# Optimization experiments

Hardware: AMD Instinct MI355X
Metric: run time of the kernel (lower is better)

Reference implementation:

```python
import jax, jax.numpy as jnp
import numpy as np

# Static architecture constants (match init_kwargs)
N, M, DIM = 2048, 4096, 256
KS = (0.9, 0.8, 0.7)
HEADS, BOT_HEADS = 4, 2
NEG_SLOPE = 0.2  # PyG GATConv default leaky-relu slope


def _p(key, shape, scale):
    return (scale * jax.random.normal(key, shape, dtype=jnp.float32))


def setup_inputs() -> dict:
    key = jax.random.key(0)
    ks = jax.random.split(key, 16)
    # Symmetric positive connectivity matrix (fMRI-like), fully dense
    R = jax.random.uniform(ks[0], (N, N), dtype=jnp.float32)
    A = 0.5 * (R + R.T)
    X = jax.random.normal(ks[1], (N, DIM), dtype=jnp.float32)
    s = 1.0 / np.sqrt(DIM).astype(np.float32)
    C, Cb = DIM // HEADS, DIM // BOT_HEADS
    inp = {
        'A': A, 'X': X,
        'W_down': _p(ks[2], (3, DIM, DIM), s),
        'as_down': _p(ks[3], (3, HEADS, C), s),
        'ad_down': _p(ks[4], (3, HEADS, C), s),
        'b_down': jnp.zeros((3, DIM), jnp.float32),
        'W_up': _p(ks[5], (3, DIM, DIM), s),
        'as_up': _p(ks[6], (3, HEADS, C), s),
        'ad_up': _p(ks[7], (3, HEADS, C), s),
        'b_up': jnp.zeros((3, DIM), jnp.float32),
        'W_bot': _p(ks[8], (DIM, DIM), s),
        'as_bot': _p(ks[9], (BOT_HEADS, Cb), s),
        'ad_bot': _p(ks[10], (BOT_HEADS, Cb), s),
        'b_bot': jnp.zeros((DIM,), jnp.float32),
        'W_pool': _p(ks[11], (3, DIM), s),
        'b_pool': jnp.zeros((3,), jnp.float32),
        'W_ups': _p(ks[12], (M, N), 1.0 / np.sqrt(N).astype(np.float32)),
        'b_ups': jnp.zeros((M,), jnp.float32),
    }
    return inp


def _sym_norm(A):
    # A_tilde = A + I ; D^{-1/2} A_tilde D^{-1/2} as elementwise broadcast
    A = A + jnp.eye(A.shape[0], dtype=A.dtype)
    d = A.sum(axis=1) + 1e-5
    di = d ** -0.5
    return di[:, None] * A * di[None, :]


def _gat(A, X, W, a_src, a_dst, b):
    # Dense-masked GATConv (concat=True, eval mode => no dropout).
    # Edge j->i exists iff A[j, i] > 0 (dense_to_sparse row=src, col=tgt).
    n = X.shape[0]
    H, C = a_src.shape
    x = (X @ W).reshape(n, H, C)                       # [n, H, C]
    s = jnp.einsum('nhc,hc->nh', x, a_src)             # source logit term
    t = jnp.einsum('nhc,hc->nh', x, a_dst)             # target logit term
    logits = jax.nn.leaky_relu(t[:, None, :] + s[None, :, :], NEG_SLOPE)  # [i, j, h]
    mask = (A.T > 0)[:, :, None]
    attn = jax.nn.softmax(jnp.where(mask, logits, -jnp.inf), axis=1)
    out = jnp.einsum('ijh,jhc->ihc', attn, x).reshape(n, H * C) + b
    return jax.nn.relu(out)


def reference(A, X, W_down, as_down, ad_down, b_down,
              W_up, as_up, ad_up, b_up,
              W_bot, as_bot, ad_bot, b_bot,
              W_pool, b_pool, W_ups, b_ups):
    A = _sym_norm(A)
    A_hist, idx_hist = [], []
    # Encoder: GAT -> top-k pool (gather rows/cols)
    for i in range(3):
        X = _gat(A, X, W_down[i], as_down[i], ad_down[i], b_down[i])
        A_hist.append(A)
        scores = jax.nn.sigmoid(X @ W_pool[i] + b_pool[i])
        k = max(2, int(KS[i] * A.shape[0]))            # static sizes
        vals, idx = jax.lax.top_k(scores, k)
        X = X[idx] * vals[:, None]
        A = A[idx][:, idx]
        idx_hist.append(idx)
    X = _gat(A, X, W_bot, as_bot, ad_bot, b_bot)
    # Decoder: scatter-unpool -> GAT -> adjacency reconstruction
    for i in range(3):
        u = 2 - i
        A, idx = A_hist[u], idx_hist[u]
        Xn = jnp.zeros((A.shape[0], X.shape[1]), X.dtype).at[idx].set(X)
        X = _gat(A, Xn, W_up[i], as_up[i], ad_up[i], b_up[i])
    # Upsampler: Linear(n->m) on X^T, then A_up = relu(Xu Xu^T)
    X_up = W_ups @ X + b_ups[:, None]                  # [M, DIM]
    A_up = jax.nn.relu(X_up @ X_up.T)                  # [M, M]
    return A_up
```

## Files before the change

### kernel.cpp

```cpp
#include <hip/hip_runtime.h>
#include <math.h>

#define NEG 0.2f
#define NMAX 2048
#define CHUNK 64
#define NCHMAX 32

__device__ __forceinline__ float lrelu(float v) { return v > 0.f ? v : NEG * v; }
__device__ __forceinline__ unsigned fenc(float v) {
    unsigned u = __float_as_uint(v);
    return (u & 0x80000000u) ? ~u : (u | 0x80000000u);
}
__device__ __forceinline__ float fdec(unsigned u) {
    return (u & 0x80000000u) ? __uint_as_float(u ^ 0x80000000u) : __uint_as_float(~u);
}

__global__ __launch_bounds__(256) void gemm_ks(const float* __restrict__ A,
                                               const float* __restrict__ B,
                                               float* __restrict__ C,
                                               const int* __restrict__ rowmapA,
                                               const float* __restrict__ rowscale,
                                               const int* __restrict__ rowmapC,
                                               int M, int N, int K) {
    __shared__ float As[16][68];
    __shared__ float Bs[16][68];
    const int tid = threadIdx.x;
    const int m0 = blockIdx.x * 64, n0 = blockIdx.y * 64;
    const int kchunk = K / gridDim.z;
    const int kbeg = blockIdx.z * kchunk, kend = kbeg + kchunk;
    const int tm = tid >> 4, tn = tid & 15;
    const int lr = tid >> 2, lc4 = (tid & 3) * 4;
    const int br = tid >> 4, bc4 = (tid & 15) * 4;
    const int am = m0 + lr;
    const bool aval = am < M;
    int arow = 0; float ascale = 1.f;
    if (aval) { arow = rowmapA ? rowmapA[am] : am; if (rowscale) ascale = rowscale[arow]; }
    const float* Ap = A + (size_t)arow * K;
    float4 va = make_float4(0.f, 0.f, 0.f, 0.f), vb;
    if (aval) va = *(const float4*)(Ap + kbeg + lc4);
    vb = *(const float4*)(B + (size_t)(kbeg + br) * N + n0 + bc4);
    float acc[4][4] = {{0.f}};
    for (int k0 = kbeg; k0 < kend; k0 += 16) {
        As[lc4 + 0][lr] = va.x * ascale; As[lc4 + 1][lr] = va.y * ascale;
        As[lc4 + 2][lr] = va.z * ascale; As[lc4 + 3][lr] = va.w * ascale;
        *(float4*)&Bs[br][bc4] = vb;
        __syncthreads();
        if (k0 + 16 < kend) {
            if (aval) va = *(const float4*)(Ap + k0 + 16 + lc4);
            vb = *(const float4*)(B + (size_t)(k0 + 16 + br) * N + n0 + bc4);
        }
#pragma unroll
        for (int kk = 0; kk < 16; ++kk) {
            float a[4], b[4];
            *(float4*)a = *(const float4*)&As[kk][tm * 4];
            *(float4*)b = *(const float4*)&Bs[kk][tn * 4];
#pragma unroll
            for (int x = 0; x < 4; ++x)
#pragma unroll
                for (int y = 0; y < 4; ++y) acc[x][y] = fmaf(a[x], b[y], acc[x][y]);
        }
        __syncthreads();
    }
#pragma unroll
    for (int x = 0; x < 4; ++x) {
        int m = m0 + tm * 4 + x;
        if (m >= M) continue;
        int orow = rowmapC ? rowmapC[m] : m;
        float* dst = C + (size_t)orow * N + n0 + tn * 4;
#pragma unroll
        for (int y = 0; y < 4; ++y) atomicAdd(dst + y, acc[x][y]);
    }
}

__global__ __launch_bounds__(256) void st_kernel(const float* __restrict__ xw,
                                                 const float* __restrict__ asrc,
                                                 const float* __restrict__ adst,
                                                 float* __restrict__ S, float* __restrict__ T,
                                                 unsigned* __restrict__ SMX,
                                                 int n, int Hh, int Cc) {
    int gid = blockIdx.x * 256 + threadIdx.x;
    int i = gid / Hh, h = gid - i * Hh;
    float s = -INFINITY;
    if (i < n) {
        const float* xr = xw + (size_t)i * 256 + h * Cc;
        const float* pa = asrc + h * Cc;
        const float* pd = adst + h * Cc;
        float sv = 0.f, tv = 0.f;
        for (int c = 0; c < Cc; c += 4) {
            float4 xv = *(const float4*)(xr + c);
            float4 av = *(const float4*)(pa + c);
            float4 dv = *(const float4*)(pd + c);
            sv += xv.x * av.x + xv.y * av.y + xv.z * av.z + xv.w * av.w;
            tv += xv.x * dv.x + xv.y * dv.y + xv.z * dv.z + xv.w * dv.w;
        }
        S[(size_t)i * Hh + h] = sv;
        T[(size_t)i * Hh + h] = tv;
        s = sv;
    }
    for (int off = Hh; off < 64; off <<= 1) s = fmaxf(s, __shfl_xor(s, off));
    int lane = threadIdx.x & 63;
    if (lane < Hh && s > -INFINITY) atomicMax(SMX + lane, fenc(s));
}

__global__ __launch_bounds__(256) void rank_k(const float* __restrict__ S,
                                              float* __restrict__ SS, int* __restrict__ PERM,
                                              int n, int Hh) {
    __shared__ float s[NMAX];
    int h = blockIdx.y;
    for (int j = threadIdx.x; j < n; j += 256) s[j] = S[(size_t)j * Hh + h];
    __syncthreads();
    int i = blockIdx.x * 256 + threadIdx.x;
    if (i >= n) return;
    float v = s[i];
    int cnt = 0, j = 0;
    for (; j + 4 <= n; j += 4) {
        float4 sv = *(const float4*)&s[j];
        cnt += (sv.x > v) || (sv.x == v && (j + 0) < i);
        cnt += (sv.y > v) || (sv.y == v && (j + 1) < i);
        cnt += (sv.z > v) || (sv.z == v && (j + 2) < i);
        cnt += (sv.w > v) || (sv.w == v && (j + 3) < i);
    }
    for (; j < n; ++j) {
        float sj = s[j];
        cnt += (sj > v) || (sj == v && j < i);
    }
    SS[h * NMAX + cnt] = v;
    PERM[h * NMAX + cnt] = i;
}

__global__ __launch_bounds__(256) void chunk_k(const float* __restrict__ XW,
                                               const float* __restrict__ SS,
                                               const int* __restrict__ PERM,
                                               const unsigned* __restrict__ SMX,
                                               float* __restrict__ TOT1, float* __restrict__ TOT2,
                                               float* __restrict__ ZT1, float* __restrict__ ZT2,
                                               int n, int Cc) {
    const int h = blockIdx.x, ch = blockIdx.y;
    const int nh = 256 / Cc, seg = CHUNK / nh;
    const int c = threadIdx.x % Cc, half = threadIdx.x / Cc;
    __shared__ float ssh[CHUNK];
    __shared__ int pjh[CHUNK];
    __shared__ float red1[256], red2[256];
    __shared__ float zr1[4], zr2[4];
    if (threadIdx.x < CHUNK) {
        int rk = ch * CHUNK + threadIdx.x;
        ssh[threadIdx.x] = (rk < n) ? SS[h * NMAX + rk] : 0.f;
        pjh[threadIdx.x] = (rk < n) ? PERM[h * NMAX + rk] : -1;
    }
    __syncthreads();
    const float smax = fdec(SMX[h]);
    float t1 = 0.f, t2 = 0.f, z1 = 0.f, z2 = 0.f;
#pragma unroll 4
    for (int q = 0; q < seg; ++q) {
        int r = half * seg + q;
        int j = pjh[r];
        if (j < 0) continue;
        float d = ssh[r] - smax;
        float w1 = expf(d), w2 = expf(NEG * d);
        float x = XW[(size_t)j * 256 + h * Cc + c];
        t1 = fmaf(w1, x, t1); t2 = fmaf(w2, x, t2);
        z1 += w1; z2 += w2;
    }
    red1[threadIdx.x] = t1; red2[threadIdx.x] = t2;
    if (c == 0) { zr1[half] = z1; zr2[half] = z2; }
    __syncthreads();
    if (half == 0) {
        for (int hh = 1; hh < nh; ++hh) { t1 += red1[hh * Cc + c]; t2 += red2[hh * Cc + c]; }
        TOT1[((size_t)h * NCHMAX + ch) * Cc + c] = t1;
        TOT2[((size_t)h * NCHMAX + ch) * Cc + c] = t2;
        if (c == 0) {
            float a = z1, b = z2;
            for (int hh = 1; hh < nh; ++hh) { a += zr1[hh]; b += zr2[hh]; }
            ZT1[h * NCHMAX + ch] = a;
            ZT2[h * NCHMAX + ch] = b;
        }
    }
}

__global__ __launch_bounds__(256) void combine_k(
    const float* __restrict__ XW, const float* __restrict__ SS,
    const int* __restrict__ PERM, const unsigned* __restrict__ SMX,
    const float* __restrict__ T,
    const float* __restrict__ TOT1, const float* __restrict__ TOT2,
    const float* __restrict__ ZT1, const float* __restrict__ ZT2,
    const float* __restrict__ bias, const float* __restrict__ Wp,
    const float* __restrict__ bp,
    float* __restrict__ Xout, float* __restrict__ SC, int n, int Hh, int nch) {
    const int i = blockIdx.x, t = threadIdx.x;
    const int C = 256 / Hh;
    __shared__ float f1s[4], f2s[4], invs[4], smaxs[4];
    __shared__ int qs[4], chs[4];
    __shared__ float coef[256];
    __shared__ int permsh[256];
    __shared__ float redw[4];
    float z1p = 0.f, z2s = 0.f;
    if (t < Hh) {
        int h = t;
        float smax = fdec(SMX[h]);
        smaxs[h] = smax;
        float tv = T[(size_t)i * Hh + h];
        float u = tv + smax, m = lrelu(u);
        f1s[h] = expf(u - m);
        f2s[h] = expf(NEG * u - m);
        float thr = -tv;
        int lo = 0, hi = n;
        while (lo < hi) {
            int mid = (lo + hi) >> 1;
            if (SS[h * NMAX + mid] > thr) lo = mid + 1; else hi = mid;
        }
        int q = lo;
        int ch = min(q / CHUNK, nch - 1);
        qs[h] = q; chs[h] = ch;
        for (int cc = 0; cc < ch; ++cc) z1p += ZT1[h * NCHMAX + cc];
        for (int cc = ch + 1; cc < nch; ++cc) z2s += ZT2[h * NCHMAX + cc];
    }
    __syncthreads();
    if (t < Hh * CHUNK) {
        int h = t >> 6, r = t & 63;
        int rank = chs[h] * CHUNK + r;
        float w = 0.f; int j = 0;
        if (rank < n) {
            float ssv = SS[h * NMAX + rank];
            j = PERM[h * NMAX + rank];
            float d = ssv - smaxs[h];
            w = (rank < qs[h]) ? f1s[h] * expf(d) : f2s[h] * expf(NEG * d);
        }
        coef[t] = w; permsh[t] = j;
    }
    __syncthreads();
    if (t < Hh) {
        int h = t;
        float den = fmaf(f1s[h], z1p, f2s[h] * z2s);
        for (int r = 0; r < CHUNK; ++r) den += coef[h * CHUNK + r];
        invs[h] = 1.f / den;
    }
    __syncthreads();
    const int h = t / C, c = t - h * C;
    const float* xcol = XW + h * C + c;
    float csum = 0.f;
#pragma unroll 8
    for (int r = 0; r < CHUNK; ++r)
        csum = fmaf(coef[h * CHUNK + r], xcol[(size_t)permsh[h * CHUNK + r] * 256], csum);
    float a1 = 0.f, a2 = 0.f;
    const int ch = chs[h];
    for (int cc = 0; cc < ch; ++cc) a1 += TOT1[((size_t)h * NCHMAX + cc) * C + c];
    for (int cc = ch + 1; cc < nch; ++cc) a2 += TOT2[((size_t)h * NCHMAX + cc) * C + c];
    float out = (fmaf(f1s[h], a1, f2s[h] * a2) + csum) * invs[h] + bias[t];
    out = fmaxf(out, 0.f);
    Xout[(size_t)i * 256 + t] = out;
    if (Wp) {
        float v = out * Wp[t];
#pragma unroll
        for (int off = 32; off; off >>= 1) v += __shfl_xor(v, off);
        if ((t & 63) == 0) redw[t >> 6] = v;
        __syncthreads();
        if (t == 0)
            SC[i] = 1.f / (1.f + expf(-(redw[0] + redw[1] + redw[2] + redw[3] + bp[0])));
    }
}

__global__ __launch_bounds__(256) void topk_k(const float* __restrict__ SC,
                                              int* __restrict__ IDX, int n, int k) {
    __shared__ float s[NMAX];
    for (int j = threadIdx.x; j < n; j += 256) s[j] = SC[j];
    __syncthreads();
    int i = blockIdx.x * 256 + threadIdx.x;
    if (i >= n) return;
    float v = s[i];
    int cnt = 0, j = 0;
    for (; j + 4 <= n; j += 4) {
        float4 sv = *(const float4*)&s[j];
        cnt += (sv.x > v) || (sv.x == v && (j + 0) < i);
        cnt += (sv.y > v) || (sv.y == v && (j + 1) < i);
        cnt += (sv.z > v) || (sv.z == v && (j + 2) < i);
        cnt += (sv.w > v) || (sv.w == v && (j + 3) < i);
    }
    for (; j < n; ++j) {
        float sj = s[j];
        cnt += (sj > v) || (sj == v && j < i);
    }
    if (cnt < k) IDX[cnt] = i;
}

__global__ __launch_bounds__(256) void ttr_sym(const float* __restrict__ A,
                                               const float* __restrict__ bias,
                                               float* __restrict__ C, int M, int K) {
    const int L = blockIdx.x;
    int by = (int)((sqrtf(8.f * L + 1.f) - 1.f) * 0.5f);
    while ((by + 1) * (by + 2) / 2 <= L) ++by;
    while (by * (by + 1) / 2 > L) --by;
    const int bx = L - by * (by + 1) / 2;
    __shared__ float As[16][132];
    __shared__ float Bs[16][132];
    const int tid = threadIdx.x;
    const int m0 = bx * 128, n0 = by * 128;
    const int lr = tid >> 1, lc8 = (tid & 1) * 8;
    const int tm = tid >> 4, tn = tid & 15;
    const float ab = bias[m0 + lr], bb = bias[n0 + lr];
    const float* Ar = A + (size_t)(m0 + lr) * K;
    const float* Br = A + (size_t)(n0 + lr) * K;
    float4 va0 = *(const float4*)(Ar + lc8), va1 = *(const float4*)(Ar + lc8 + 4);
    float4 vb0 = *(const float4*)(Br + lc8), vb1 = *(const float4*)(Br + lc8 + 4);
    float acc[8][8] = {{0.f}};
    for (int k0 = 0; k0 < K; k0 += 16) {
        As[lc8 + 0][lr] = va0.x + ab; As[lc8 + 1][lr] = va0.y + ab;
        As[lc8 + 2][lr] = va0.z + ab; As[lc8 + 3][lr] = va0.w + ab;
        As[lc8 + 4][lr] = va1.x + ab; As[lc8 + 5][lr] = va1.y + ab;
        As[lc8 + 6][lr] = va1.z + ab; As[lc8 + 7][lr] = va1.w + ab;
        Bs[lc8 + 0][lr] = vb0.x + bb; Bs[lc8 + 1][lr] = vb0.y + bb;
        Bs[lc8 + 2][lr] = vb0.z + bb; Bs[lc8 + 3][lr] = vb0.w + bb;
        Bs[lc8 + 4][lr] = vb1.x + bb; Bs[lc8 + 5][lr] = vb1.y + bb;
        Bs[lc8 + 6][lr] = vb1.z + bb; Bs[lc8 + 7][lr] = vb1.w + bb;
        __syncthreads();
        if (k0 + 16 < K) {
            va0 = *(const float4*)(Ar + k0 + 16 + lc8); va1 = *(const float4*)(Ar + k0 + 20 + lc8);
            vb0 = *(const float4*)(Br + k0 + 16 + lc8); vb1 = *(const float4*)(Br + k0 + 20 + lc8);
        }
#pragma unroll
        for (int kk = 0; kk < 16; ++kk) {
            float a[8], b[8];
            *(float4*)&a[0] = *(const float4*)&As[kk][tm * 4];
            *(float4*)&a[4] = *(const float4*)&As[kk][64 + tm * 4];
            *(float4*)&b[0] = *(const float4*)&Bs[kk][tn * 4];
            *(float4*)&b[4] = *(const float4*)&Bs[kk][64 + tn * 4];
#pragma unroll
            for (int x = 0; x < 8; ++x)
#pragma unroll
                for (int y = 0; y < 8; ++y) acc[x][y] = fmaf(a[x], b[y], acc[x][y]);
        }
        __syncthreads();
    }
#pragma unroll
    for (int x = 0; x < 8; ++x)
#pragma unroll
        for (int y = 0; y < 8; ++y) acc[x][y] = fmaxf(acc[x][y], 0.f);
#pragma unroll
    for (int x = 0; x < 8; ++x) {
        int row = m0 + ((x < 4) ? tm * 4 + x : 64 + tm * 4 + (x - 4));
        float* dst = C + (size_t)row * M + n0;
        *(float4*)(dst + tn * 4) = make_float4(acc[x][0], acc[x][1], acc[x][2], acc[x][3]);
        *(float4*)(dst + 64 + tn * 4) = make_float4(acc[x][4], acc[x][5], acc[x][6], acc[x][7]);
    }
    if (bx != by) {
#pragma unroll
        for (int y = 0; y < 8; ++y) {
            int row = n0 + ((y < 4) ? tn * 4 + y : 64 + tn * 4 + (y - 4));
            float* dst = C + (size_t)row * M + m0;
            *(float4*)(dst + tm * 4) = make_float4(acc[0][y], acc[1][y], acc[2][y], acc[3][y]);
            *(float4*)(dst + 64 + tm * 4) = make_float4(acc[4][y], acc[5][y], acc[6][y], acc[7][y]);
        }
    }
}

extern "C" void kernel_launch(void* const* d_in, const int* in_sizes, int n_in,
                              void* d_out, int out_size, void* d_ws, size_t ws_size,
                              hipStream_t stream) {
    const float* X0      = (const float*)d_in[1];
    const float* W_down  = (const float*)d_in[2];
    const float* as_down = (const float*)d_in[3];
    const float* ad_down = (const float*)d_in[4];
    const float* b_down  = (const float*)d_in[5];
    const float* W_up    = (const float*)d_in[6];
    const float* as_up   = (const float*)d_in[7];
    const float* ad_up   = (const float*)d_in[8];
    const float* b_up    = (const float*)d_in[9];
    const float* W_bot   = (const float*)d_in[10];
    const float* as_bot  = (const float*)d_in[11];
    const float* ad_bot  = (const float*)d_in[12];
    const float* b_bot   = (const float*)d_in[13];
    const float* W_pool  = (const float*)d_in[14];
    const float* b_pool  = (const float*)d_in[15];
    const float* W_ups   = (const float*)d_in[16];
    const float* b_ups   = (const float*)d_in[17];
    float* out = (float*)d_out;

    float* F = (float*)d_ws;
    size_t o = 0;
    float* Xb  = F + o; o += 2048 * 256;
    float* XW  = F + o; o += 2048 * 256;
    unsigned* SMX = (unsigned*)(F + o); o += 16;
    float* S   = F + o; o += 2048 * 4;
    float* T   = F + o; o += 2048 * 4;
    float* SS  = F + o; o += 2048 * 4;
    int* PERM  = (int*)(F + o); o += 2048 * 4;
    float* TOT1 = F + o; o += 8192;
    float* TOT2 = F + o; o += 8192;
    float* ZT1 = F + o; o += 128;
    float* ZT2 = F + o; o += 128;
    float* SC  = F + o; o += 2048;
    int* IDXs[3];
    IDXs[0] = (int*)(F + o); o += 2048;
    IDXs[1] = (int*)(F + o); o += 2048;
    IDXs[2] = (int*)(F + o); o += 2048;
    float* XU  = F + o; o += 4096 * 256;

    auto cdiv = [](int a, int b) { return (a + b - 1) / b; };

    auto run_gat = [&](const float* Xin, int Mrows, int n, const float* W,
                       const float* asrc, const float* adst, const float* bias, int Hh,
                       const int* rmA, const float* rscale, const int* rmC,
                       const float* Wp, const float* bp) {
        int C = 256 / Hh;
        int nch = cdiv(n, CHUNK);
        hipMemsetAsync(XW, 0, (size_t)(2048 * 256 + 16) * 4, stream);
        gemm_ks<<<dim3(cdiv(Mrows, 64), 4, 4), 256, 0, stream>>>(Xin, W, XW, rmA, rscale,
                                                                 rmC, Mrows, 256, 256);
        st_kernel<<<cdiv(n * Hh, 256), 256, 0, stream>>>(XW, asrc, adst, S, T, SMX, n, Hh, C);
        rank_k<<<dim3(cdiv(n, 256), Hh), 256, 0, stream>>>(S, SS, PERM, n, Hh);
        chunk_k<<<dim3(Hh, nch), 256, 0, stream>>>(XW, SS, PERM, SMX, TOT1, TOT2, ZT1, ZT2,
                                                   n, C);
        combine_k<<<n, 256, 0, stream>>>(XW, SS, PERM, SMX, T, TOT1, TOT2, ZT1, ZT2, bias,
                                         Wp, bp, Xb, SC, n, Hh, nch);
    };

    const int ns[4] = {2048, 1843, 1474, 1031};

    for (int l = 0; l < 3; ++l) {
        int n = ns[l], k = ns[l + 1];
        run_gat(l ? Xb : X0, n, n, W_down + (size_t)l * 65536, as_down + l * 256,
                ad_down + l * 256, b_down + l * 256, 4,
                l ? IDXs[l - 1] : nullptr, l ? SC : nullptr, nullptr,
                W_pool + l * 256, b_pool + l);
        topk_k<<<cdiv(n, 256), 256, 0, stream>>>(SC, IDXs[l], n, k);
    }

    run_gat(Xb, ns[3], ns[3], W_bot, as_bot, ad_bot, b_bot, 2, IDXs[2], SC, nullptr,
            nullptr, nullptr);

    for (int i = 0; i < 3; ++i) {
        int u = 2 - i;
        int pn = ns[u], kc = ns[u + 1];
        run_gat(Xb, kc, pn, W_up + (size_t)i * 65536, as_up + i * 256, ad_up + i * 256,
                b_up + i * 256, 4, nullptr, nullptr, IDXs[u], nullptr, nullptr);
    }

    hipMemsetAsync(XU, 0, (size_t)4096 * 256 * 4, stream);
    gemm_ks<<<dim3(64, 4, 4), 256, 0, stream>>>(W_ups, Xb, XU, nullptr, nullptr, nullptr,
                                                4096, 256, 2048);
    ttr_sym<<<528, 256, 0, stream>>>(XU, b_ups, out, 4096, 256);
}
```

Before: 1.183 ms.

## Fuse each GAT layer and upsampler into persistent kernels with grid barriers

Replaces the per-layer sequence of gemm, score, rank, chunk and combine launches, plus the top-k and memsets, with one persistent kernel per GAT layer that uses software grid-wide barriers between phases. The up-path scatter is replaced by an inverse-index gather. S/T logit computation is fused into the GEMM epilogue, and split-K atomics are replaced by direct stores. Softmax max now comes from the sorted array instead of an atomic max. The upsampler GEMM and the symmetric relu(XXᵀ) are also fused into a single persistent kernel with larger 128x128 tiles. This aims to cut launch overhead and memset/atomic traffic, at the risk of deadlock if not all 512 blocks are co-resident, and barrier spin cost.

After: 3.206 ms. +171.1%, slower.

```diff
diff --git a/kernel.cpp b/kernel.cpp
--- a/kernel.cpp
+++ b/kernel.cpp
@@ -5,349 +5,447 @@
 #define NMAX 2048
 #define CHUNK 64
 #define NCHMAX 32
+#define GRID 512
 
 __device__ __forceinline__ float lrelu(float v) { return v > 0.f ? v : NEG * v; }
-__device__ __forceinline__ unsigned fenc(float v) {
-    unsigned u = __float_as_uint(v);
-    return (u & 0x80000000u) ? ~u : (u | 0x80000000u);
+
+__device__ __forceinline__ void gsync(unsigned* c, unsigned nb) {
+    __syncthreads();
+    if (threadIdx.x == 0) {
+        __threadfence();
+        atomicAdd(c, 1u);
+        while (__hip_atomic_load(c, __ATOMIC_ACQUIRE, __HIP_MEMORY_SCOPE_AGENT) < nb) {
+            __builtin_amdgcn_s_sleep(2);
+        }
+        __threadfence();
+    }
+    __syncthreads();
 }
-__device__ __forceinline__ float fdec(unsigned u) {
-    return (u & 0x80000000u) ? __uint_as_float(u ^ 0x80000000u) : __uint_as_float(~u);
+
+struct GatArgs {
+    const float* Xin; const float* W; float* XW;
+    const int* rowmapA; const float* rowscale;
+    const float* asrc; const float* adst;
+    float* S; float* T; float* SS; int* PERM;
+    float* TOT1; float* TOT2; float* ZT1; float* ZT2;
+    const float* bias; const float* Wp; const float* bp;
+    float* Xout; float* SC;
+    const float* tkSC; int* tkIDX; int* tkINV; int tkN; int tkK;
+    unsigned* bar;
+    int n; int Hh;
+};
+
+union SharedU {
+    struct { float As[16][68], Bs[16][68], Sred[64][17], Tred[64][17]; } g;
+    struct { float s[NMAX]; } rk;
+    struct { float ssh[CHUNK]; int pjh[CHUNK]; float red1[256], red2[256], zr1[4], zr2[4]; } ck;
+    struct { float f1s[4], f2s[4], invs[4], smaxs[4]; int qs[4], chs[4];
+             float coef[256]; int permsh[256]; float redw[4]; } cb;
+    struct { float sc[NMAX]; } tk;
+};
+
+__global__ __launch_bounds__(256, 2) void gat_fused(GatArgs a) {
+    __shared__ SharedU sh;
+    const int tid = threadIdx.x;
+    const int nb = gridDim.x, bid = blockIdx.x;
+    const int n = a.n, Hh = a.Hh, Cc = 256 / Hh;
+    unsigned* bar = a.bar;
+    int slot = 0;
+
+    if (a.tkIDX) {
+        for (int base = bid * 256; base < a.tkN; base += nb * 256) {
+            for (int j = tid; j < a.tkN; j += 256) sh.tk.sc[j] = a.tkSC[j];
+            __syncthreads();
+            int i = base + tid;
+            if (i < a.tkN) {
+                float v = sh.tk.sc[i];
+                int cnt = 0, j = 0;
+                for (; j + 4 <= a.tkN; j += 4) {
+                    float4 sv = *(const float4*)&sh.tk.sc[j];
+                    cnt += (sv.x > v) || (sv.x == v && (j + 0) < i);
+                    cnt += (sv.y > v) || (sv.y == v && (j + 1) < i);
+                    cnt += (sv.z > v) || (sv.z == v && (j + 2) < i);
+                    cnt += (sv.w > v) || (sv.w == v && (j + 3) < i);
+                }
+                for (; j < a.tkN; ++j) {
+                    float sj = sh.tk.sc[j];
+                    cnt += (sj > v) || (sj == v && j < i);
+                }
+                if (cnt < a.tkK) { a.tkIDX[cnt] = i; a.tkINV[i] = cnt; }
+                else a.tkINV[i] = -1;
+            }
+            __syncthreads();
+        }
+    }
+    gsync(bar + slot++, nb);
+
+    {
+        const int mt = (n + 63) >> 6;
+        for (int tt = bid; tt < mt * 4; tt += nb) {
+            const int m0 = (tt >> 2) * 64, n0 = (tt & 3) * 64;
+            const int tm = tid >> 4, tn = tid & 15;
+            const int lr = tid >> 2, lc4 = (tid & 3) * 4;
+            const int br = tid >> 4, bc4 = (tid & 15) * 4;
+            const int am = m0 + lr;
+            bool aval = am < n;
+            int arow = am; float ascale = 1.f;
+            if (aval && a.rowmapA) { arow = a.rowmapA[am]; if (arow < 0) { aval = false; arow = 0; } }
+            if (aval && a.rowscale) ascale = a.rowscale[arow];
+            const float* Ap = a.Xin + (size_t)arow * 256;
+            float4 va = make_float4(0.f, 0.f, 0.f, 0.f);
+            if (aval) va = *(const float4*)(Ap + lc4);
+            float4 vb = *(const float4*)(a.W + (size_t)br * 256 + n0 + bc4);
+            float acc[4][4] = {{0.f}};
+            for (int k0 = 0; k0 < 256; k0 += 16) {
+                sh.g.As[lc4 + 0][lr] = va.x * ascale; sh.g.As[lc4 + 1][lr] = va.y * ascale;
+                sh.g.As[lc4 + 2][lr] = va.z * ascale; sh.g.As[lc4 + 3][lr] = va.w * ascale;
+                *(float4*)&sh.g.Bs[br][bc4] = vb;
+                __syncthreads();
+                if (k0 + 16 < 256) {
+                    if (aval) va = *(const float4*)(Ap + k0 + 16 + lc4);
+                    vb = *(const float4*)(a.W + (size_t)(k0 + 16 + br) * 256 + n0 + bc4);
+                }
+#pragma unroll
+                for (int kk = 0; kk < 16; ++kk) {
+                    float aa[4], bb[4];
+                    *(float4*)aa = *(const float4*)&sh.g.As[kk][tm * 4];
+                    *(float4*)bb = *(const float4*)&sh.g.Bs[kk][tn * 4];
+#pragma unroll
+                    for (int x = 0; x < 4; ++x)
+#pragma unroll
+                        for (int y = 0; y < 4; ++y) acc[x][y] = fmaf(aa[x], bb[y], acc[x][y]);
+                }
+                __syncthreads();
+            }
+#pragma unroll
+            for (int x = 0; x < 4; ++x) {
+                int m = m0 + tm * 4 + x;
+                if (m < n)
+                    *(float4*)(a.XW + (size_t)m * 256 + n0 + tn * 4) =
+                        make_float4(acc[x][0], acc[x][1], acc[x][2], acc[x][3]);
+            }
+            if (Hh == 4) {
+                const int h = tt & 3;
+                float4 a4 = *(const float4*)(a.asrc + h * 64 + tn * 4);
+                float4 d4 = *(const float4*)(a.adst + h * 64 + tn * 4);
+#pragma unroll
+                for (int x = 0; x < 4; ++x) {
+                    sh.g.Sred[tm * 4 + x][tn] = acc[x][0] * a4.x + acc[x][1] * a4.y +
+                                                acc[x][2] * a4.z + acc[x][3] * a4.w;
+                    sh.g.Tred[tm * 4 + x][tn] = acc[x][0] * d4.x + acc[x][1] * d4.y +
+                                                acc[x][2] * d4.z + acc[x][3] * d4.w;
+                }
+                __syncthreads();
+                if (tid < 64) {
+                    int m = m0 + tid;
+                    if (m < n) {
+                        float s = 0.f, t = 0.f;
+#pragma unroll
+                        for (int q = 0; q < 16; ++q) { s += sh.g.Sred[tid][q]; t += sh.g.Tred[tid][q]; }
+                        a.S[(size_t)m * Hh + h] = s;
+                        a.T[(size_t)m * Hh + h] = t;
+                    }
+                }
+                __syncthreads();
+            }
+        }
+    }
+    gsync(bar + slot++, nb);
+
+    if (Hh == 2) {
+        for (int gid = bid * 256 + tid; gid < n * 2; gid += nb * 256) {
+            int i = gid >> 1, h = gid & 1;
+            const float* xr = a.XW + (size_t)i * 256 + h * 128;
+            const float* pa = a.asrc + h * 128;
+            const float* pd = a.adst + h * 128;
+            float sv = 0.f, tv = 0.f;
+            for (int c = 0; c < 128; c += 4) {
+                float4 xv = *(const float4*)(xr + c);
+                float4 av = *(const float4*)(pa + c);
+                float4 dv = *(const float4*)(pd + c);
+                sv += xv.x * av.x + xv.y * av.y + xv.z * av.z + xv.w * av.w;
+                tv += xv.x * dv.x + xv.y * dv.y + xv.z * dv.z + xv.w * dv.w;
+            }
+            a.S[(size_t)i * 2 + h] = sv;
+            a.T[(size_t)i * 2 + h] = tv;
+        }
+        gsync(bar + slot++, nb);
+    }
+
+    {
+        const int nseg = (n + 255) >> 8;
+        for (int w = bid; w < Hh * nseg; w += nb) {
+            const int h = w / nseg, seg = w - h * nseg;
+            for (int j = tid; j < n; j += 256) sh.rk.s[j] = a.S[(size_t)j * Hh + h];
+            __syncthreads();
+            int i = seg * 256 + tid;
+            if (i < n) {
+                float v = sh.rk.s[i];
+                int cnt = 0, j = 0;
+                for (; j + 4 <= n; j += 4) {
+                    float4 sv = *(const float4*)&sh.rk.s[j];
+                    cnt += (sv.x > v) || (sv.x == v && (j + 0) < i);
+                    cnt += (sv.y > v) || (sv.y == v && (j + 1) < i);
+                    cnt += (sv.z > v) || (sv.z == v && (j + 2) < i);
+                    cnt += (sv.w > v) || (sv.w == v && (j + 3) < i);
+                }
+                for (; j < n; ++j) {
+                    float sj = sh.rk.s[j];
+                    cnt += (sj > v) || (sj == v && j < i);
+                }
+                a.SS[h * NMAX + cnt] = v;
+                a.PERM[h * NMAX + cnt] = i;
+            }
+            __syncthreads();
+        }
+    }
+    gsync(bar + slot++, nb);
+
+    {
+        const int nch = (n + CHUNK - 1) / CHUNK;
+        for (int w = bid; w < Hh * nch; w += nb) {
+            const int h = w / nch, ch = w - h * nch;
+            const int nh = 256 / Cc, seg2 = CHUNK / nh;
+            const int c = tid % Cc, half = tid / Cc;
+            if (tid < CHUNK) {
+                int rk2 = ch * CHUNK + tid;
+                sh.ck.ssh[tid] = (rk2 < n) ? a.SS[h * NMAX + rk2] : 0.f;
+                sh.ck.pjh[tid] = (rk2 < n) ? a.PERM[h * NMAX + rk2] : -1;
+            }
+            __syncthreads();
+            const float smax = a.SS[h * NMAX];
+            float t1 = 0.f, t2 = 0.f, z1 = 0.f, z2 = 0.f;
+            for (int q = 0; q < seg2; ++q) {
+                int r = half * seg2 + q;
+                int j = sh.ck.pjh[r];
+                if (j < 0) continue;
+                float d = sh.ck.ssh[r] - smax;
+                float w1 = expf(d), w2 = expf(NEG * d);
+                float x = a.XW[(size_t)j * 256 + h * Cc + c];
+                t1 = fmaf(w1, x, t1); t2 = fmaf(w2, x, t2);
+                z1 += w1; z2 += w2;
+            }
+            sh.ck.red1[tid] = t1; sh.ck.red2[tid] = t2;
+            if (c == 0) { sh.ck.zr1[half] = z1; sh.ck.zr2[half] = z2; }
+            __syncthreads();
+            if (half == 0) {
+                for (int hh = 1; hh < nh; ++hh) { t1 += sh.ck.red1[hh * Cc + c]; t2 += sh.ck.red2[hh * Cc + c]; }
+                a.TOT1[((size_t)h * NCHMAX + ch) * Cc + c] = t1;
+                a.TOT2[((size_t)h * NCHMAX + ch) * Cc + c] = t2;
+                if (c == 0) {
+                    float za = z1, zb = z2;
+                    for (int hh = 1; hh < nh; ++hh) { za += sh.ck.zr1[hh]; zb += sh.ck.zr2[hh]; }
+                    a.ZT1[h * NCHMAX + ch] = za;
+                    a.ZT2[h * NCHMAX + ch] = zb;
+                }
+            }
+            __syncthreads();
+        }
+    }
+    gsync(bar + slot++, nb);
+
+    {
+        const int nch = (n + CHUNK - 1) / CHUNK;
+        for (int i = bid; i < n; i += nb) {
+            const int t = tid;
+            float z1p = 0.f, z2s = 0.f;
+            if (t < Hh) {
+                int h = t;
+                float smax = a.SS[h * NMAX];
+                sh.cb.smaxs[h] = smax;
+                float tv = a.T[(size_t)i * Hh + h];
+                float u = tv + smax, m = lrelu(u);
+                sh.cb.f1s[h] = expf(u - m);
+                sh.cb.f2s[h] = expf(NEG * u - m);
+                float thr = -tv;
+                int lo = 0, hi = n;
+                while (lo < hi) {
+                    int mid = (lo + hi) >> 1;
+                    if (a.SS[h * NMAX + mid] > thr) lo = mid + 1; else hi = mid;
+                }
+                int q = lo;
+                int ch = min(q / CHUNK, nch - 1);
+                sh.cb.qs[h] = q; sh.cb.chs[h] = ch;
+                for (int cc = 0; cc < ch; ++cc) z1p += a.ZT1[h * NCHMAX + cc];
+                for (int cc = ch + 1; cc < nch; ++cc) z2s += a.ZT2[h * NCHMAX + cc];
+            }
+            __syncthreads();
+            if (t < Hh * CHUNK) {
+                int h = t >> 6, r = t & 63;
+                int rank = sh.cb.chs[h] * CHUNK + r;
+                float w = 0.f; int j = 0;
+                if (rank < n) {
+                    float ssv = a.SS[h * NMAX + rank];
+                    j = a.PERM[h * NMAX + rank];
+                    float d = ssv - sh.cb.smaxs[h];
+                    w = (rank < sh.cb.qs[h]) ? sh.cb.f1s[h] * expf(d)
+                                             : sh.cb.f2s[h] * expf(NEG * d);
+                }
+                sh.cb.coef[t] = w; sh.cb.permsh[t] = j;
+            }
+            __syncthreads();
+            if (t < Hh) {
+                int h = t;
+                float den = fmaf(sh.cb.f1s[h], z1p, sh.cb.f2s[h] * z2s);
+                for (int r = 0; r < CHUNK; ++r) den += sh.cb.coef[h * CHUNK + r];
+                sh.cb.invs[h] = 1.f / den;
+            }
+            __syncthreads();
+            const int h = t / Cc, c = t - h * Cc;
+            const float* xcol = a.XW + h * Cc + c;
+            float csum = 0.f;
+#pragma unroll 8
+            for (int r = 0; r < CHUNK; ++r)
+                csum = fmaf(sh.cb.coef[h * CHUNK + r],
+                            xcol[(size_t)sh.cb.permsh[h * CHUNK + r] * 256], csum);
+            float a1 = 0.f, a2 = 0.f;
+            const int ch = sh.cb.chs[h];
+            for (int cc = 0; cc < ch; ++cc) a1 += a.TOT1[((size_t)h * NCHMAX + cc) * Cc + c];
+            for (int cc = ch + 1; cc < nch; ++cc) a2 += a.TOT2[((size_t)h * NCHMAX + cc) * Cc + c];
+            float out = (fmaf(sh.cb.f1s[h], a1, sh.cb.f2s[h] * a2) + csum) * sh.cb.invs[h] + a.bias[t];
+            out = fmaxf(out, 0.f);
+            a.Xout[(size_t)i * 256 + t] = out;
+            if (a.Wp) {
+                float v = out * a.Wp[t];
+#pragma unroll
+                for (int off = 32; off; off >>= 1) v += __shfl_xor(v, off);
+                if ((t & 63) == 0) sh.cb.redw[t >> 6] = v;
+                __syncthreads();
+                if (t == 0)
+                    a.SC[i] = 1.f / (1.f + expf(-(sh.cb.redw[0] + sh.cb.redw[1] +
+                                                  sh.cb.redw[2] + sh.cb.redw[3] + a.bp[0])));
+            }
+            __syncthreads();
+        }
+    }
 }
 
-__global__ __launch_bounds__(256) void gemm_ks(const float* __restrict__ A,
-                                               const float* __restrict__ B,
-                                               float* __restrict__ C,
-                                               const int* __restrict__ rowmapA,
-                                               const float* __restrict__ rowscale,
-                                               const int* __restrict__ rowmapC,
-                                               int M, int N, int K) {
-    __shared__ float As[16][68];
-    __shared__ float Bs[16][68];
+struct UpsArgs {
+    const float* Wu; const float* Xb; float* XU; float* slabB;
+    const float* bups; float* out; unsigned* bar;
+};
+
+union UpsShared {
+    struct { float As[16][68], Bs[16][68]; } p0;
+    struct { float As[16][132], Bs[16][132]; } p2;
+};
+
+__global__ __launch_bounds__(256, 2) void ups_fused(UpsArgs a) {
+    __shared__ UpsShared sh;
     const int tid = threadIdx.x;
-    const int m0 = blockIdx.x * 64, n0 = blockIdx.y * 64;
-    const int kchunk = K / gridDim.z;
-    const int kbeg = blockIdx.z * kchunk, kend = kbeg + kchunk;
-    const int tm = tid >> 4, tn = tid & 15;
-    const int lr = tid >> 2, lc4 = (tid & 3) * 4;
-    const int br = tid >> 4, bc4 = (tid & 15) * 4;
-    const int am = m0 + lr;
-    const bool aval = am < M;
-    int arow = 0; float ascale = 1.f;
-    if (aval) { arow = rowmapA ? rowmapA[am] : am; if (rowscale) ascale = rowscale[arow]; }
-    const float* Ap = A + (size_t)arow * K;
-    float4 va = make_float4(0.f, 0.f, 0.f, 0.f), vb;
-    if (aval) va = *(const float4*)(Ap + kbeg + lc4);
-    vb = *(const float4*)(B + (size_t)(kbeg + br) * N + n0 + bc4);
-    float acc[4][4] = {{0.f}};
-    for (int k0 = kbeg; k0 < kend; k0 += 16) {
-        As[lc4 + 0][lr] = va.x * ascale; As[lc4 + 1][lr] = va.y * ascale;
-        As[lc4 + 2][lr] = va.z * ascale; As[lc4 + 3][lr] = va.w * ascale;
-        *(float4*)&Bs[br][bc4] = vb;
-        __syncthreads();
-        if (k0 + 16 < kend) {
-            if (aval) va = *(const float4*)(Ap + k0 + 16 + lc4);
-            vb = *(const float4*)(B + (size_t)(k0 + 16 + br) * N + n0 + bc4);
-        }
-#pragma unroll
-        for (int kk = 0; kk < 16; ++kk) {
-            float a[4], b[4];
-            *(float4*)a = *(const float4*)&As[kk][tm * 4];
-            *(float4*)b = *(const float4*)&Bs[kk][tn * 4];
-#pragma unroll
-            for (int x = 0; x < 4; ++x)
-#pragma unroll
-                for (int y = 0; y < 4; ++y) acc[x][y] = fmaf(a[x], b[y], acc[x][y]);
-        }
-        __syncthreads();
-    }
-#pragma unroll
-    for (int x = 0; x < 4; ++x) {
-        int m = m0 + tm * 4 + x;
-        if (m >= M) continue;
-        int orow = rowmapC ? rowmapC[m] : m;
-        float* dst = C + (size_t)orow * N + n0 + tn * 4;
-#pragma unroll
-        for (int y = 0; y < 4; ++y) atomicAdd(dst + y, acc[x][y]);
-    }
-}
-
-__global__ __launch_bounds__(256) void st_kernel(const float* __restrict__ xw,
-                                                 const float* __restrict__ asrc,
-                                                 const float* __restrict__ adst,
-                                                 float* __restrict__ S, float* __restrict__ T,
-                                                 unsigned* __restrict__ SMX,
-                                                 int n, int Hh, int Cc) {
-    int gid = blockIdx.x * 256 + threadIdx.x;
-    int i = gid / Hh, h = gid - i * Hh;
-    float s = -INFINITY;
-    if (i < n) {
-        const float* xr = xw + (size_t)i * 256 + h * Cc;
-        const float* pa = asrc + h * Cc;
-        const float* pd = adst + h * Cc;
-        float sv = 0.f, tv = 0.f;
-        for (int c = 0; c < Cc; c += 4) {
-            float4 xv = *(const float4*)(xr + c);
-            float4 av = *(const float4*)(pa + c);
-            float4 dv = *(const float4*)(pd + c);
-            sv += xv.x * av.x + xv.y * av.y + xv.z * av.z + xv.w * av.w;
-            tv += xv.x * dv.x + xv.y * dv.y + xv.z * dv.z + xv.w * dv.w;
-        }
-        S[(size_t)i * Hh + h] = sv;
-        T[(size_t)i * Hh + h] = tv;
-        s = sv;
-    }
-    for (int off = Hh; off < 64; off <<= 1) s = fmaxf(s, __shfl_xor(s, off));
-    int lane = threadIdx.x & 63;
-    if (lane < Hh && s > -INFINITY) atomicMax(SMX + lane, fenc(s));
-}
-
-__global__ __launch_bounds__(256) void rank_k(const float* __restrict__ S,
-                                              float* __restrict__ SS, int* __restrict__ PERM,
-                                              int n, int Hh) {
-    __shared__ float s[NMAX];
-    int h = blockIdx.y;
-    for (int j = threadIdx.x; j < n; j += 256) s[j] = S[(size_t)j * Hh + h];
-    __syncthreads();
-    int i = blockIdx.x * 256 + threadIdx.x;
-    if (i >= n) return;
-    float v = s[i];
-    int cnt = 0, j = 0;
-    for (; j + 4 <= n; j += 4) {
-        float4 sv = *(const float4*)&s[j];
-        cnt += (sv.x > v) || (sv.x == v && (j + 0) < i);
-        cnt += (sv.y > v) || (sv.y == v && (j + 1) < i);
-        cnt += (sv.z > v) || (sv.z == v && (j + 2) < i);
-        cnt += (sv.w > v) || (sv.w == v && (j + 3) < i);
-    }
-    for (; j < n; ++j) {
-        float sj = s[j];
-        cnt += (sj > v) || (sj == v && j < i);
-    }
-    SS[h * NMAX + cnt] = v;
-    PERM[h * NMAX + cnt] = i;
-}
-
-__global__ __launch_bounds__(256) void chunk_k(const float* __restrict__ XW,
-                                               const float* __restrict__ SS,
-                                               const int* __restrict__ PERM,
-                                               const unsigned* __restrict__ SMX,
-                                               float* __restrict__ TOT1, float* __restrict__ TOT2,
-                                               float* __restrict__ ZT1, float* __restrict__ ZT2,
-                                               int n, int Cc) {
-    const int h = blockIdx.x, ch = blockIdx.y;
-    const int nh = 256 / Cc, seg = CHUNK / nh;
-    const int c = threadIdx.x % Cc, half = threadIdx.x / Cc;
-    __shared__ float ssh[CHUNK];
-    __shared__ int pjh[CHUNK];
-    __shared__ float red1[256], red2[256];
-    __shared__ float zr1[4], zr2[4];
-    if (threadIdx.x < CHUNK) {
-        int rk = ch * CHUNK + threadIdx.x;
-        ssh[threadIdx.x] = (rk < n) ? SS[h * NMAX + rk] : 0.f;
-        pjh[threadIdx.x] = (rk < n) ? PERM[h * NMAX + rk] : -1;
-    }
-    __syncthreads();
-    const float smax = fdec(SMX[h]);
-    float t1 = 0.f, t2 = 0.f, z1 = 0.f, z2 = 0.f;
-#pragma unroll 4
-    for (int q = 0; q < seg; ++q) {
-        int r = half * seg + q;
-        int j = pjh[r];
-        if (j < 0) continue;
-        float d = ssh[r] - smax;
-        float w1 = expf(d), w2 = expf(NEG * d);
-        float x = XW[(size_t)j * 256 + h * Cc + c];
-        t1 = fmaf(w1, x, t1); t2 = fmaf(w2, x, t2);
-        z1 += w1; z2 += w2;
-    }
-    red1[threadIdx.x] = t1; red2[threadIdx.x] = t2;
-    if (c == 0) { zr1[half] = z1; zr2[half] = z2; }
-    __syncthreads();
-    if (half == 0) {
-        for (int hh = 1; hh < nh; ++hh) { t1 += red1[hh * Cc + c]; t2 += red2[hh * Cc + c]; }
-        TOT1[((size_t)h * NCHMAX + ch) * Cc + c] = t1;
-        TOT2[((size_t)h * NCHMAX + ch) * Cc + c] = t2;
-        if (c == 0) {
-            float a = z1, b = z2;
-            for (int hh = 1; hh < nh; ++hh) { a += zr1[hh]; b += zr2[hh]; }
-            ZT1[h * NCHMAX + ch] = a;
-            ZT2[h * NCHMAX + ch] = b;
-        }
-    }
-}
-
-__global__ __launch_bounds__(256) void combine_k(
-    const float* __restrict__ XW, const float* __restrict__ SS,
-    const int* __restrict__ PERM, const unsigned* __restrict__ SMX,
-    const float* __restrict__ T,
-    const float* __restrict__ TOT1, const float* __restrict__ TOT2,
-    const float* __restrict__ ZT1, const float* __restrict__ ZT2,
-    const float* __restrict__ bias, const float* __restrict__ Wp,
-    const float* __restrict__ bp,
-    float* __restrict__ Xout, float* __restrict__ SC, int n, int Hh, int nch) {
-    const int i = blockIdx.x, t = threadIdx.x;
-    const int C = 256 / Hh;
-    __shared__ float f1s[4], f2s[4], invs[4], smaxs[4];
-    __shared__ int qs[4], chs[4];
-    __shared__ float coef[256];
-    __shared__ int permsh[256];
-    __shared__ float redw[4];
-    float z1p = 0.f, z2s = 0.f;
-    if (t < Hh) {
-        int h = t;
-        float smax = fdec(SMX[h]);
-        smaxs[h] = smax;
-        float tv = T[(size_t)i * Hh + h];
-        float u = tv + smax, m = lrelu(u);
-        f1s[h] = expf(u - m);
-        f2s[h] = expf(NEG * u - m);
-        float thr = -tv;
-        int lo = 0, hi = n;
-        while (lo < hi) {
-            int mid = (lo + hi) >> 1;
-            if (SS[h * NMAX + mid] > thr) lo = mid + 1; else hi = mid;
-        }
-        int q = lo;
-        int ch = min(q / CHUNK, nch - 1);
-        qs[h] = q; chs[h] = ch;
-        for (int cc = 0; cc < ch; ++cc) z1p += ZT1[h * NCHMAX + cc];
-        for (int cc = ch + 1; cc < nch; ++cc) z2s += ZT2[h * NCHMAX + cc];
-    }
-    __syncthreads();
-    if (t < Hh * CHUNK) {
-        int h = t >> 6, r = t & 63;
-        int rank = chs[h] * CHUNK + r;
-        float w = 0.f; int j = 0;
-        if (rank < n) {
-            float ssv = SS[h * NMAX + rank];
-            j = PERM[h * NMAX + rank];
-            float d = ssv - smaxs[h];
-            w = (rank < qs[h]) ? f1s[h] * expf(d) : f2s[h] * expf(NEG * d);
-        }
-        coef[t] = w; permsh[t] = j;
-    }
-    __syncthreads();
-    if (t < Hh) {
-        int h = t;
-        float den = fmaf(f1s[h], z1p, f2s[h] * z2s);
-        for (int r = 0; r < CHUNK; ++r) den += coef[h * CHUNK + r];
-        invs[h] = 1.f / den;
-    }
-    __syncthreads();
-    const int h = t / C, c = t - h * C;
-    const float* xcol = XW + h * C + c;
-    float csum = 0.f;
-#pragma unroll 8
-    for (int r = 0; r < CHUNK; ++r)
-        csum = fmaf(coef[h * CHUNK + r], xcol[(size_t)permsh[h * CHUNK + r] * 256], csum);
-    float a1 = 0.f, a2 = 0.f;
-    const int ch = chs[h];
-    for (int cc = 0; cc < ch; ++cc) a1 += TOT1[((size_t)h * NCHMAX + cc) * C + c];
-    for (int cc = ch + 1; cc < nch; ++cc) a2 += TOT2[((size_t)h * NCHMAX + cc) * C + c];
-    float out = (fmaf(f1s[h], a1, f2s[h] * a2) + csum) * invs[h] + bias[t];
-    out = fmaxf(out, 0.f);
-    Xout[(size_t)i * 256 + t] = out;
-    if (Wp) {
-        float v = out * Wp[t];
-#pragma unroll
-        for (int off = 32; off; off >>= 1) v += __shfl_xor(v, off);
-        if ((t & 63) == 0) redw[t >> 6] = v;
-        __syncthreads();
-        if (t == 0)
-            SC[i] = 1.f / (1.f + expf(-(redw[0] + redw[1] + redw[2] + redw[3] + bp[0])));
-    }
-}
-
-__global__ __launch_bounds__(256) void topk_k(const float* __restrict__ SC,
-                                              int* __restrict__ IDX, int n, int k) {
-    __shared__ float s[NMAX];
-    for (int j = threadIdx.x; j < n; j += 256) s[j] = SC[j];
-    __syncthreads();
-    int i = blockIdx.x * 256 + threadIdx.x;
-    if (i >= n) return;
-    float v = s[i];
-    int cnt = 0, j = 0;
-    for (; j + 4 <= n; j += 4) {
-        float4 sv = *(const float4*)&s[j];
-        cnt += (sv.x > v) || (sv.x == v && (j + 0) < i);
-        cnt += (sv.y > v) || (sv.y == v && (j + 1) < i);
-        cnt += (sv.z > v) || (sv.z == v && (j + 2) < i);
-        cnt += (sv.w > v) || (sv.w == v && (j + 3) < i);
-    }
-    for (; j < n; ++j) {
-        float sj = s[j];
-        cnt += (sj > v) || (sj == v && j < i);
-    }
-    if (cnt < k) IDX[cnt] = i;
-}
-
-__global__ __launch_bounds__(256) void ttr_sym(const float* __restrict__ A,
-                                               const float* __restrict__ bias,
-                                               float* __restrict__ C, int M, int K) {
-    const int L = blockIdx.x;
-    int by = (int)((sqrtf(8.f * L + 1.f) - 1.f) * 0.5f);
-    while ((by + 1) * (by + 2) / 2 <= L) ++by;
-    while (by * (by + 1) / 2 > L) --by;
-    const int bx = L - by * (by + 1) / 2;
-    __shared__ float As[16][132];
-    __shared__ float Bs[16][132];
-    const int tid = threadIdx.x;
-    const int m0 = bx * 128, n0 = by * 128;
+    const int bid = blockIdx.x, nb = gridDim.x;
+
+    for (int w = bid; w < 512; w += nb) {
+        const int z = w >> 8, rem = w & 255;
+        const int m0 = (rem >> 2) * 64, n0 = (rem & 3) * 64;
+        const int kbeg = z * 1024, kend = kbeg + 1024;
+        const int tm = tid >> 4, tn = tid & 15;
+        const int lr = tid >> 2, lc4 = (tid & 3) * 4;
+        const int br = tid >> 4, bc4 = (tid & 15) * 4;
+        const float* Ap = a.Wu + (size_t)(m0 + lr) * 2048;
+        float4 va = *(const float4*)(Ap + kbeg + lc4);
+        float4 vb = *(const float4*)(a.Xb + (size_t)(kbeg + br) * 256 + n0 + bc4);
+        float acc[4][4] = {{0.f}};
+        for (int k0 = kbeg; k0 < kend; k0 += 16) {
+            sh.p0.As[lc4 + 0][lr] = va.x; sh.p0.As[lc4 + 1][lr] = va.y;
+            sh.p0.As[lc4 + 2][lr] = va.z; sh.p0.As[lc4 + 3][lr] = va.w;
+            *(float4*)&sh.p0.Bs[br][bc4] = vb;
+            __syncthreads();
+            if (k0 + 16 < kend) {
+                va = *(const float4*)(Ap + k0 + 16 + lc4);
+                vb = *(const float4*)(a.Xb + (size_t)(k0 + 16 + br) * 256 + n0 + bc4);
+            }
+#pragma unroll
+            for (int kk = 0; kk < 16; ++kk) {
+                float aa[4], bb[4];
+                *(float4*)aa = *(const float4*)&sh.p0.As[kk][tm * 4];
+                *(float4*)bb = *(const float4*)&sh.p0.Bs[kk][tn * 4];
+#pragma unroll
+                for (int x = 0; x < 4; ++x)
+#pragma unroll
+                    for (int y = 0; y < 4; ++y) acc[x][y] = fmaf(aa[x], bb[y], acc[x][y]);
+            }
+            __syncthreads();
+        }
+        float* base = (z == 0) ? a.XU : a.slabB;
+#pragma unroll
+        for (int x = 0; x < 4; ++x)
+            *(float4*)(base + (size_t)(m0 + tm * 4 + x) * 256 + n0 + tn * 4) =
+                make_float4(acc[x][0], acc[x][1], acc[x][2], acc[x][3]);
+    }
+    gsync(a.bar + 0, nb);
+
+    {
+        float4* xu4 = (float4*)a.XU;
+        const float4* sb4 = (const float4*)a.slabB;
+        for (int i = bid * 256 + tid; i < 4096 * 256 / 4; i += nb * 256) {
+            float4 v = xu4[i], w = sb4[i];
+            xu4[i] = make_float4(v.x + w.x, v.y + w.y, v.z + w.z, v.w + w.w);
+        }
+    }
+    gsync(a.bar + 1, nb);
+
     const int lr = tid >> 1, lc8 = (tid & 1) * 8;
     const int tm = tid >> 4, tn = tid & 15;
-    const float ab = bias[m0 + lr], bb = bias[n0 + lr];
-    const float* Ar = A + (size_t)(m0 + lr) * K;
-    const float* Br = A + (size_t)(n0 + lr) * K;
-    float4 va0 = *(const float4*)(Ar + lc8), va1 = *(const float4*)(Ar + lc8 + 4);
-    float4 vb0 = *(const float4*)(Br + lc8), vb1 = *(const float4*)(Br + lc8 + 4);
-    float acc[8][8] = {{0.f}};
-    for (int k0 = 0; k0 < K; k0 += 16) {
-        As[lc8 + 0][lr] = va0.x + ab; As[lc8 + 1][lr] = va0.y + ab;
-        As[lc8 + 2][lr] = va0.z + ab; As[lc8 + 3][lr] = va0.w + ab;
-        As[lc8 + 4][lr] = va1.x + ab; As[lc8 + 5][lr] = va1.y + ab;
-        As[lc8 + 6][lr] = va1.z + ab; As[lc8 + 7][lr] = va1.w + ab;
-        Bs[lc8 + 0][lr] = vb0.x + bb; Bs[lc8 + 1][lr] = vb0.y + bb;
-        Bs[lc8 + 2][lr] = vb0.z + bb; Bs[lc8 + 3][lr] = vb0.w + bb;
-        Bs[lc8 + 4][lr] = vb1.x + bb; Bs[lc8 + 5][lr] = vb1.y + bb;
-        Bs[lc8 + 6][lr] = vb1.z + bb; Bs[lc8 + 7][lr] = vb1.w + bb;
-        __syncthreads();
-        if (k0 + 16 < K) {
-            va0 = *(const float4*)(Ar + k0 + 16 + lc8); va1 = *(const float4*)(Ar + k0 + 20 + lc8);
-            vb0 = *(const float4*)(Br + k0 + 16 + lc8); vb1 = *(const float4*)(Br + k0 + 20 + lc8);
-        }
-#pragma unroll
-        for (int kk = 0; kk < 16; ++kk) {
-            float a[8], b[8];
-            *(float4*)&a[0] = *(const float4*)&As[kk][tm * 4];
-            *(float4*)&a[4] = *(const float4*)&As[kk][64 + tm * 4];
-            *(float4*)&b[0] = *(const float4*)&Bs[kk][tn * 4];
-            *(float4*)&b[4] = *(const float4*)&Bs[kk][64 + tn * 4];
-#pragma unroll
-            for (int x = 0; x < 8; ++x)
-#pragma unroll
-                for (int y = 0; y < 8; ++y) acc[x][y] = fmaf(a[x], b[y], acc[x][y]);
-        }
-        __syncthreads();
-    }
-#pragma unroll
-    for (int x = 0; x < 8; ++x)
-#pragma unroll
-        for (int y = 0; y < 8; ++y) acc[x][y] = fmaxf(acc[x][y], 0.f);
-#pragma unroll
-    for (int x = 0; x < 8; ++x) {
-        int row = m0 + ((x < 4) ? tm * 4 + x : 64 + tm * 4 + (x - 4));
-        float* dst = C + (size_t)row * M + n0;
-        *(float4*)(dst + tn * 4) = make_float4(acc[x][0], acc[x][1], acc[x][2], acc[x][3]);
-        *(float4*)(dst + 64 + tn * 4) = make_float4(acc[x][4], acc[x][5], acc[x][6], acc[x][7]);
-    }
-    if (bx != by) {
-#pragma unroll
-        for (int y = 0; y < 8; ++y) {
-            int row = n0 + ((y < 4) ? tn * 4 + y : 64 + tn * 4 + (y - 4));
-            float* dst = C + (size_t)row * M + m0;
-            *(float4*)(dst + tm * 4) = make_float4(acc[0][y], acc[1][y], acc[2][y], acc[3][y]);
-            *(float4*)(dst + 64 + tm * 4) = make_float4(acc[4][y], acc[5][y], acc[6][y], acc[7][y]);
+    for (int L = bid; L < 528; L += nb) {
+        int by = (int)((sqrtf(8.f * L + 1.f) - 1.f) * 0.5f);
+        while ((by + 1) * (by + 2) / 2 <= L) ++by;
+        while (by * (by + 1) / 2 > L) --by;
+        const int bx = L - by * (by + 1) / 2;
+        const int m0 = bx * 128, n0 = by * 128;
+        const float ab = a.bups[m0 + lr], bb2 = a.bups[n0 + lr];
+        const float* Ar = a.XU + (size_t)(m0 + lr) * 256;
+        const float* Br = a.XU + (size_t)(n0 + lr) * 256;
+        float4 va0 = *(const float4*)(Ar + lc8), va1 = *(const float4*)(Ar + lc8 + 4);
+        float4 vb0 = *(const float4*)(Br + lc8), vb1 = *(const float4*)(Br + lc8 + 4);
+        float acc[8][8] = {{0.f}};
+        for (int k0 = 0; k0 < 256; k0 += 16) {
+            sh.p2.As[lc8 + 0][lr] = va0.x + ab; sh.p2.As[lc8 + 1][lr] = va0.y + ab;
+            sh.p2.As[lc8 + 2][lr] = va0.z + ab; sh.p2.As[lc8 + 3][lr] = va0.w + ab;
+            sh.p2.As[lc8 + 4][lr] = va1.x + ab; sh.p2.As[lc8 + 5][lr] = va1.y + ab;
+            sh.p2.As[lc8 + 6][lr] = va1.z + ab; sh.p2.As[lc8 + 7][lr] = va1.w + ab;
+            sh.p2.Bs[lc8 + 0][lr] = vb0.x + bb2; sh.p2.Bs[lc8 + 1][lr] = vb0.y + bb2;
+            sh.p2.Bs[lc8 + 2][lr] = vb0.z + bb2; sh.p2.Bs[lc8 + 3][lr] = vb0.w + bb2;
+            sh.p2.Bs[lc8 + 4][lr] = vb1.x + bb2; sh.p2.Bs[lc8 + 5][lr] = vb1.y + bb2;
+            sh.p2.Bs[lc8 + 6][lr] = vb1.z + bb2; sh.p2.Bs[lc8 + 7][lr] = vb1.w + bb2;
+            __syncthreads();
+            if (k0 + 16 < 256) {
+                va0 = *(const float4*)(Ar + k0 + 16 + lc8); va1 = *(const float4*)(Ar + k0 + 20 + lc8);
+                vb0 = *(const float4*)(Br + k0 + 16 + lc8); vb1 = *(const float4*)(Br + k0 + 20 + lc8);
+            }
+#pragma unroll
+            for (int kk = 0; kk < 16; ++kk) {
+                float aa[8], bb[8];
+                *(float4*)&aa[0] = *(const float4*)&sh.p2.As[kk][tm * 4];
+                *(float4*)&aa[4] = *(const float4*)&sh.p2.As[kk][64 + tm * 4];
+                *(float4*)&bb[0] = *(const float4*)&sh.p2.Bs[kk][tn * 4];
+                *(float4*)&bb[4] = *(const float4*)&sh.p2.Bs[kk][64 + tn * 4];
+#pragma unroll
+                for (int x = 0; x < 8; ++x)
+#pragma unroll
+                    for (int y = 0; y < 8; ++y) acc[x][y] = fmaf(aa[x], bb[y], acc[x][y]);
+            }
+            __syncthreads();
+        }
+#pragma unroll
+        for (int x = 0; x < 8; ++x)
+#pragma unroll
+            for (int y = 0; y < 8; ++y) acc[x][y] = fmaxf(acc[x][y], 0.f);
+#pragma unroll
+        for (int x = 0; x < 8; ++x) {
+            int row = m0 + ((x < 4) ? tm * 4 + x : 64 + tm * 4 + (x - 4));
+            float* dst = a.out + (size_t)row * 4096 + n0;
+            *(float4*)(dst + tn * 4) = make_float4(acc[x][0], acc[x][1], acc[x][2], acc[x][3]);
+            *(float4*)(dst + 64 + tn * 4) = make_float4(acc[x][4], acc[x][5], acc[x][6], acc[x][7]);
+        }
+        if (bx != by) {
+#pragma unroll
+            for (int y = 0; y < 8; ++y) {
+                int row = n0 + ((y < 4) ? tn * 4 + y : 64 + tn * 4 + (y - 4));
+                float* dst = a.out + (size_t)row * 4096 + m0;
+                *(float4*)(dst + tm * 4) = make_float4(acc[0][y], acc[1][y], acc[2][y], acc[3][y]);
+                *(float4*)(dst + 64 + tm * 4) = make_float4(acc[4][y], acc[5][y], acc[6][y], acc[7][y]);
+            }
         }
     }
 }
@@ -378,7 +476,6 @@
     size_t o = 0;
     float* Xb  = F + o; o += 2048 * 256;
     float* XW  = F + o; o += 2048 * 256;
-    unsigned* SMX = (unsigned*)(F + o); o += 16;
     float* S   = F + o; o += 2048 * 4;
     float* T   = F + o; o += 2048 * 4;
     float* SS  = F + o; o += 2048 * 4;
@@ -388,54 +485,59 @@
     float* ZT1 = F + o; o += 128;
     float* ZT2 = F + o; o += 128;
     float* SC  = F + o; o += 2048;
-    int* IDXs[3];
+    int* IDXs[3]; int* INVs[3];
     IDXs[0] = (int*)(F + o); o += 2048;
     IDXs[1] = (int*)(F + o); o += 2048;
     IDXs[2] = (int*)(F + o); o += 2048;
-    float* XU  = F + o; o += 4096 * 256;
-
-    auto cdiv = [](int a, int b) { return (a + b - 1) / b; };
-
-    auto run_gat = [&](const float* Xin, int Mrows, int n, const float* W,
-                       const float* asrc, const float* adst, const float* bias, int Hh,
-                       const int* rmA, const float* rscale, const int* rmC,
-                       const float* Wp, const float* bp) {
-        int C = 256 / Hh;
-        int nch = cdiv(n, CHUNK);
-        hipMemsetAsync(XW, 0, (size_t)(2048 * 256 + 16) * 4, stream);
-        gemm_ks<<<dim3(cdiv(Mrows, 64), 4, 4), 256, 0, stream>>>(Xin, W, XW, rmA, rscale,
-                                                                 rmC, Mrows, 256, 256);
-        st_kernel<<<cdiv(n * Hh, 256), 256, 0, stream>>>(XW, asrc, adst, S, T, SMX, n, Hh, C);
-        rank_k<<<dim3(cdiv(n, 256), Hh), 256, 0, stream>>>(S, SS, PERM, n, Hh);
-        chunk_k<<<dim3(Hh, nch), 256, 0, stream>>>(XW, SS, PERM, SMX, TOT1, TOT2, ZT1, ZT2,
-                                                   n, C);
-        combine_k<<<n, 256, 0, stream>>>(XW, SS, PERM, SMX, T, TOT1, TOT2, ZT1, ZT2, bias,
-                                         Wp, bp, Xb, SC, n, Hh, nch);
+    INVs[0] = (int*)(F + o); o += 2048;
+    INVs[1] = (int*)(F + o); o += 2048;
+    INVs[2] = (int*)(F + o); o += 2048;
+    unsigned* BAR = (unsigned*)(F + o); o += 64;
+    float* XU    = F + o; o += 4096 * 256;
+    float* SLABB = F + o; o += 4096 * 256;
+
+    hipMemsetAsync(BAR, 0, 64 * sizeof(unsigned), stream);
+
+    const int ns[4] = {2048, 1843, 1474, 1031};
+    int launch_id = 0;
+
+    auto launch_gat = [&](const float* Xin, int n, const float* W,
+                          const float* asrc, const float* adst, const float* bias, int Hh,
+                          const int* rmA, const float* rscale,
+                          const float* Wp, const float* bp,
+                          const float* tkSC, int* tkIDX, int* tkINV, int tkN, int tkK) {
+        GatArgs ga;
+        ga.Xin = Xin; ga.W = W; ga.XW = XW;
+        ga.rowmapA = rmA; ga.rowscale = rscale;
+        ga.asrc = asrc; ga.adst = adst;
+        ga.S = S; ga.T = T; ga.SS = SS; ga.PERM = PERM;
+        ga.TOT1 = TOT1; ga.TOT2 = TOT2; ga.ZT1 = ZT1; ga.ZT2 = ZT2;
+        ga.bias = bias; ga.Wp = Wp; ga.bp = bp;
+        ga.Xout = Xb; ga.SC = SC;
+        ga.tkSC = tkSC; ga.tkIDX = tkIDX; ga.tkINV = tkINV; ga.tkN = tkN; ga.tkK = tkK;
+        ga.bar = BAR + launch_id * 7;
+        ga.n = n; ga.Hh = Hh;
+        ++launch_id;
+        gat_fused<<<GRID, 256, 0, stream>>>(ga);
     };
 
-    const int ns[4] = {2048, 1843, 1474, 1031};
-
-    for (int l = 0; l < 3; ++l) {
-        int n = ns[l], k = ns[l + 1];
-        run_gat(l ? Xb : X0, n, n, W_down + (size_t)l * 65536, as_down + l * 256,
-                ad_down + l * 256, b_down + l * 256, 4,
-                l ? IDXs[l - 1] : nullptr, l ? SC : nullptr, nullptr,
-                W_pool + l * 256, b_pool + l);
-        topk_k<<<cdiv(n, 256), 256, 0, stream>>>(SC, IDXs[l], n, k);
-    }
-
-    run_gat(Xb, ns[3], ns[3], W_bot, as_bot, ad_bot, b_bot, 2, IDXs[2], SC, nullptr,
-            nullptr, nullptr);
-
-    for (int i = 0; i < 3; ++i) {
-        int u = 2 - i;
-        int pn = ns[u], kc = ns[u + 1];
-        run_gat(Xb, kc, pn, W_up + (size_t)i * 65536, as_up + i * 256, ad_up + i * 256,
-                b_up + i * 256, 4, nullptr, nullptr, IDXs[u], nullptr, nullptr);
-    }
-
-    hipMemsetAsync(XU, 0, (size_t)4096 * 256 * 4, stream);
-    gemm_ks<<<dim3(64, 4, 4), 256, 0, stream>>>(W_ups, Xb, XU, nullptr, nullptr, nullptr,
-                                                4096, 256, 2048);
-    ttr_sym<<<528, 256, 0, stream>>>(XU, b_ups, out, 4096, 256);
+    launch_gat(X0, ns[0], W_down, as_down, ad_down, b_down, 4,
+               nullptr, nullptr, W_pool, b_pool, nullptr, nullptr, nullptr, 0, 0);
+    launch_gat(Xb, ns[1], W_down + 65536, as_down + 256, ad_down + 256, b_down + 256, 4,
+               IDXs[0], SC, W_pool + 256, b_pool + 1, SC, IDXs[0], INVs[0], ns[0], ns[1]);
+    launch_gat(Xb, ns[2], W_down + 131072, as_down + 512, ad_down + 512, b_down + 512, 4,
+               IDXs[1], SC, W_pool + 512, b_pool + 2, SC, IDXs[1], INVs[1], ns[1], ns[2]);
+    launch_gat(Xb, ns[3], W_bot, as_bot, ad_bot, b_bot, 2,
+               IDXs[2], SC, nullptr, nullptr, SC, IDXs[2], INVs[2], ns[2], ns[3]);
+    launch_gat(Xb, ns[2], W_up, as_up, ad_up, b_up, 4,
+               INVs[2], nullptr, nullptr, nullptr, nullptr, nullptr, nullptr, 0, 0);
+    launch_gat(Xb, ns[1], W_up + 65536, as_up + 256, ad_up + 256, b_up + 256, 4,
+               INVs[1], nullptr, nullptr, nullptr, nullptr, nullptr, nullptr, 0, 0);
+    launch_gat(Xb, ns[0], W_up + 131072, as_up + 512, ad_up + 512, b_up + 512, 4,
+               INVs[0], nullptr, nullptr, nullptr, nullptr, nullptr, nullptr, 0, 0);
+
+    UpsArgs ua;
+    ua.Wu = W_ups; ua.Xb = Xb; ua.XU = XU; ua.slabB = SLABB;
+    ua.bups = b_ups; ua.out = out; ua.bar = BAR + 56;
+    ups_fused<<<GRID, 256, 0, stream>>>(ua);
 }
```
